# Optimization experiments

Measured on AMD Instinct MI355X. Metric: run time of the kernel, lower is better.

The kernel has to match this reference:

```python
import jax, jax.numpy as jnp
import numpy as np
from jax import lax

B, H, W = 1, 128, 128
KS = 3
N = KS * KS  # 9 deformable sampling points
BN_EPS = 1e-5


def conv2d(x, w, padding=0, stride=1):
    return lax.conv_general_dilated(x, w, (stride, stride),
                                    [(padding, padding), (padding, padding)],
                                    dimension_numbers=('NCHW', 'OIHW', 'NCHW'))


def bn_eval(x, gamma, beta, mean, var):
    scale = gamma / jnp.sqrt(var + BN_EPS)
    return x * scale[None, :, None, None] + (beta - mean * scale)[None, :, None, None]


def upsample_bilinear_ac(x, oh, ow):
    # F.interpolate(mode='bilinear', align_corners=True), separable gather
    b, c, h, w = x.shape
    ys = jnp.linspace(0.0, h - 1.0, oh)
    xs = jnp.linspace(0.0, w - 1.0, ow)
    y0 = jnp.floor(ys).astype(jnp.int32)
    y1 = jnp.minimum(y0 + 1, h - 1)
    wy = (ys - y0).astype(x.dtype)[None, None, :, None]
    x0 = jnp.floor(xs).astype(jnp.int32)
    x1 = jnp.minimum(x0 + 1, w - 1)
    wx = (xs - x0).astype(x.dtype)
    r = x[:, :, y0, :] * (1.0 - wy) + x[:, :, y1, :] * wy
    return r[:, :, :, x0] * (1.0 - wx) + r[:, :, :, x1] * wx


def deform_conv(x, p_w, p_b, dc_w, pad=1):
    # DeformConv2d(inc, outc, ks=3, padding=1, modulation=False):
    # offsets from a 3x3 conv, bilinear gather at p0 + p_n + offset on the
    # zero-padded input, then 3x3 kernel contraction over the 9 samples.
    b, c, h, w = x.shape
    off = conv2d(x, p_w, padding=1) + p_b[None, :, None, None]  # (b, 2N, h, w)
    rng = jnp.arange(KS, dtype=x.dtype) - (KS - 1) // 2          # [-1, 0, 1]
    pnx, pny = jnp.meshgrid(rng, rng, indexing='ij')
    # absolute sampling coords in padded frame, (b, h, w, N)
    px = jnp.transpose(off[:, :N], (0, 2, 3, 1)) + pnx.ravel() + jnp.arange(1, h + 1, dtype=x.dtype)[None, :, None, None]
    py = jnp.transpose(off[:, N:], (0, 2, 3, 1)) + pny.ravel() + jnp.arange(1, w + 1, dtype=x.dtype)[None, None, :, None]
    Hp, Wp = h + 2 * pad, w + 2 * pad
    xp = jnp.pad(x, ((0, 0), (0, 0), (pad, pad), (pad, pad))).reshape(b, c, Hp * Wp)
    fx = jnp.floor(px)
    fy = jnp.floor(py)
    x0f = jnp.clip(fx, 0, Hp - 1)
    x1f = jnp.clip(fx + 1.0, 0, Hp - 1)
    y0f = jnp.clip(fy, 0, Wp - 1)
    y1f = jnp.clip(fy + 1.0, 0, Wp - 1)
    pxc = jnp.clip(px, 0, Hp - 1)
    pyc = jnp.clip(py, 0, Wp - 1)

    def gather(qxf, qyf):
        idx = (qxf.astype(jnp.int32) * Wp + qyf.astype(jnp.int32)).reshape(b, 1, h * w * N)
        g = jnp.take_along_axis(xp, jnp.broadcast_to(idx, (b, c, h * w * N)), axis=2)
        return g.reshape(b, c, h, w, N)

    g_lt = (1.0 + (x0f - pxc)) * (1.0 + (y0f - pyc))
    g_rb = (1.0 - (x1f - pxc)) * (1.0 - (y1f - pyc))
    g_lb = (1.0 + (x0f - pxc)) * (1.0 - (y1f - pyc))
    g_rt = (1.0 - (x1f - pxc)) * (1.0 + (y0f - pyc))
    x_off = (g_lt[:, None] * gather(x0f, y0f) + g_rb[:, None] * gather(x1f, y1f)
             + g_lb[:, None] * gather(x0f, y1f) + g_rt[:, None] * gather(x1f, y0f))
    # conv(kernel=3, stride=3) on the rearranged samples == contraction over N
    return jnp.einsum('bchwk,ock->bohw', x_off, dc_w.reshape(dc_w.shape[0], c, N))


def _forward(x, low_level_feat, fm_w, fs_w, p_w, p_b, dc_w,
             lc1_w, bn1_gamma, bn1_beta, bn1_mean, bn1_var,
             lc2_w, bn2_gamma, bn2_beta, bn2_mean, bn2_var):
    xu = upsample_bilinear_ac(x, H, W)                       # (B,256,128,128)
    Z = low_level_feat                                       # AdaptiveAvgPool2d((128,128)) is identity on 128x128 input
    v = jax.nn.sigmoid(jnp.einsum('oc,bchw->bohw', fm_w, Z))
    u = jnp.einsum('bchk,bckw->bchw', low_level_feat, v) + low_level_feat
    Cf = jnp.einsum('oc,bchw->bohw', fs_w, u)
    cc = jnp.concatenate([xu, Cf], axis=1)                   # (B,512,128,128)
    fam = deform_conv(cc, p_w, p_b, dc_w) + Cf
    up1 = jax.nn.relu(bn_eval(conv2d(fam, lc1_w, padding=1), bn1_gamma, bn1_beta, bn1_mean, bn1_var))
    up2 = jax.nn.relu(bn_eval(conv2d(up1, lc2_w, padding=1), bn2_gamma, bn2_beta, bn2_mean, bn2_var))
    return up1, up2


def setup_inputs():
    key = jax.random.key(0)
    ks = jax.random.split(key, 12)
    f32 = jnp.float32
    return {
        'x': jax.random.normal(ks[0], (B, 256, 32, 32), f32),
        'low_level_feat': jax.random.normal(ks[1], (B, 256, H, W), f32),
        'fm_w': jax.random.normal(ks[2], (256, 256), f32) * 0.0625,
        'fs_w': jax.random.normal(ks[3], (256, 256), f32) * 0.0625,
        'p_w': jax.random.normal(ks[4], (2 * N, 512, 3, 3), f32) * 0.01,
        'p_b': jnp.zeros((2 * N,), f32),
        'dc_w': jax.random.normal(ks[5], (256, 512, 3, 3), f32) * 0.02,
        'lc1_w': jax.random.normal(ks[6], (256, 256, 3, 3), f32) * 0.02,
        'bn1_gamma': jnp.ones((256,), f32),
        'bn1_beta': jnp.zeros((256,), f32),
        'bn1_mean': jax.random.normal(ks[7], (256,), f32) * 0.1,
        'bn1_var': jax.random.uniform(ks[8], (256,), f32) + 0.5,
        'lc2_w': jax.random.normal(ks[9], (256, 256, 3, 3), f32) * 0.02,
        'bn2_gamma': jnp.ones((256,), f32),
        'bn2_beta': jnp.zeros((256,), f32),
        'bn2_mean': jax.random.normal(ks[10], (256,), f32) * 0.1,
        'bn2_var': jax.random.uniform(ks[11], (256,), f32) + 0.5,
    }


def reference(x, low_level_feat, fm_w, fs_w, p_w, p_b, dc_w,
              lc1_w, bn1_gamma, bn1_beta, bn1_mean, bn1_var,
              lc2_w, bn2_gamma, bn2_beta, bn2_mean, bn2_var):
    return _forward(x, low_level_feat, fm_w, fs_w, p_w, p_b, dc_w,
                    lc1_w, bn1_gamma, bn1_beta, bn1_mean, bn1_var,
                    lc2_w, bn2_gamma, bn2_beta, bn2_mean, bn2_var)
```

## Files before the change

### kernel.cpp

```cpp
#include <hip/hip_runtime.h>
#include <math.h>

#define HW   16384
#define PS   16900

typedef __attribute__((ext_vector_type(8))) short bf16x8;
typedef __attribute__((ext_vector_type(4))) float f32x4;

__device__ inline unsigned short f2bf(float x) {
    unsigned int u = __float_as_uint(x);
    unsigned int r = (u + 0x7fffu + ((u >> 16) & 1u)) >> 16;
    return (unsigned short)r;
}
__device__ inline float bf2f(unsigned short h) {
    return __uint_as_float(((unsigned int)h) << 16);
}

__global__ __launch_bounds__(256) void zero_ringP_k(unsigned short* __restrict__ base) {
    int t = blockIdx.x * 256 + threadIdx.x;
    if (t >= 520 * 32) return;
    int ck = (t & 31) << 3, rp = t >> 5;
    int row, col;
    if (rp < 130)      { row = 0;   col = rp; }
    else if (rp < 260) { row = 129; col = rp - 130; }
    else {
        int rem = rp - 260;
        if (rem >= 256) return;
        row = 1 + (rem >> 1); col = (rem & 1) ? 129 : 0;
    }
    bf16x8 z = (bf16x8){0, 0, 0, 0, 0, 0, 0, 0};
    *(bf16x8*)(base + (size_t)(row * 130 + col) * 256 + ck) = z;
}

__global__ __launch_bounds__(256) void ringT_k(unsigned short* __restrict__ ccT) {
    int t = blockIdx.x * 256 + threadIdx.x;
    if (t >= 520 * 256) return;
    int ci = t & 255, rp = t >> 8;
    int row, col;
    if (rp < 130)      { row = 0;   col = rp; }
    else if (rp < 260) { row = 129; col = rp - 130; }
    else {
        int rem = rp - 260;
        if (rem >= 256) return;
        row = 1 + (rem >> 1); col = (rem & 1) ? 129 : 0;
    }
    ccT[(size_t)(row * 130 + col) * 512 + 256 + ci] = 0;
}

__global__ __launch_bounds__(256) void upsample_k(const float* __restrict__ x,
                                                  float* __restrict__ ccpad) {
    int c = blockIdx.y;
    int idx = blockIdx.x * 256 + threadIdx.x;
    if (idx >= PS) return;
    int r = idx / 130, s = idx - r * 130;
    float val = 0.0f;
    if (r >= 1 && r <= 128 && s >= 1 && s <= 128) {
        int i = r - 1, j = s - 1;
        float yf = (float)i * (31.0f / 127.0f);
        float xf = (float)j * (31.0f / 127.0f);
        int y0 = min((int)yf, 31); int y1 = min(y0 + 1, 31);
        int x0 = min((int)xf, 31); int x1 = min(x0 + 1, 31);
        float wy = yf - (float)y0, wx = xf - (float)x0;
        const float* xc = x + (size_t)c * 1024;
        float a = xc[y0 * 32 + x0] * (1.0f - wx) + xc[y0 * 32 + x1] * wx;
        float b = xc[y1 * 32 + x0] * (1.0f - wx) + xc[y1 * 32 + x1] * wx;
        val = a * (1.0f - wy) + b * wy;
    }
    ccpad[(size_t)c * PS + idx] = val;
}

__global__ __launch_bounds__(256) void cvtT_flat_k(const float* __restrict__ src,
                                                   unsigned short* __restrict__ dst,
                                                   int npx) {
    int t = blockIdx.x * 256 + threadIdx.x;
    int c = t & 255, pix = t >> 8;
    dst[t] = f2bf(src[(size_t)c * npx + pix]);
}

__global__ __launch_bounds__(256) void cvtT_k(const float* __restrict__ src,
                                              unsigned short* __restrict__ dst) {
    int t = blockIdx.x * 256 + threadIdx.x;
    int c = t & 255, pix = t >> 8;
    dst[(size_t)pix * 512 + c] = f2bf(src[(size_t)c * PS + pix]);
}

__global__ __launch_bounds__(256) void w2bf_k(const float* __restrict__ a,
                                              const float* __restrict__ b,
                                              unsigned short* __restrict__ da,
                                              unsigned short* __restrict__ db) {
    int t = blockIdx.x * 256 + threadIdx.x;
    if (t >= 65536) return;
    da[t] = f2bf(a[t]);
    db[t] = f2bf(b[t]);
}

__global__ __launch_bounds__(256) void u_matmul_k(const float* __restrict__ llf,
                                                  const float* __restrict__ v,
                                                  float* __restrict__ u) {
    int c = blockIdx.y;
    const float* L = llf + (size_t)c * HW;
    const float* V = v   + (size_t)c * HW;
    float*       U = u   + (size_t)c * HW;
    int tid = threadIdx.x;
    int ty = tid >> 4, tx = tid & 15;
    int r0 = (blockIdx.x << 6) + (ty << 2);
    int w0 = tx << 3;
    float acc[4][8] = {};
    for (int k = 0; k < 128; ++k) {
        float a[4];
#pragma unroll
        for (int i = 0; i < 4; ++i) a[i] = L[(r0 + i) * 128 + k];
        float4 b0 = *(const float4*)(V + k * 128 + w0);
        float4 b1 = *(const float4*)(V + k * 128 + w0 + 4);
        float bv[8] = {b0.x, b0.y, b0.z, b0.w, b1.x, b1.y, b1.z, b1.w};
#pragma unroll
        for (int i = 0; i < 4; ++i)
#pragma unroll
            for (int j = 0; j < 8; ++j) acc[i][j] += a[i] * bv[j];
    }
#pragma unroll
    for (int i = 0; i < 4; ++i) {
#pragma unroll
        for (int j = 0; j < 8; ++j) acc[i][j] += L[(r0 + i) * 128 + w0 + j];
        *(float4*)(U + (r0 + i) * 128 + w0)     = make_float4(acc[i][0], acc[i][1], acc[i][2], acc[i][3]);
        *(float4*)(U + (r0 + i) * 128 + w0 + 4) = make_float4(acc[i][4], acc[i][5], acc[i][6], acc[i][7]);
    }
}

__global__ __launch_bounds__(256) void tr_dcwF9_k(const float* __restrict__ w,
                                                  unsigned short* __restrict__ dst) {
    int t = blockIdx.x * 256 + threadIdx.x;
    if (t >= 1179648) return;
    int e    = t & 7;
    int lane = (t >> 3) & 63;
    int f    = t >> 9;
    int mi   = f & 1;
    int s    = (f >> 1) & 1;
    int wv   = (f >> 2) & 7;
    int ch   = f >> 5;
    int kt   = ch >> 3;
    int o = (wv << 5) + (mi << 4) + (lane & 15);
    int c = ((ch & 7) << 6) + (s << 5) + ((lane >> 4) << 3) + e;
    dst[t] = f2bf(w[(size_t)o * 4608 + c * 9 + kt]);
}

__global__ __launch_bounds__(256) void tr_lcF_k(const float* __restrict__ w,
                                                unsigned short* __restrict__ dst) {
    int t = blockIdx.x * 256 + threadIdx.x;
    if (t >= 589824) return;
    int e    = t & 7;
    int lane = (t >> 3) & 63;
    int mi   = (t >> 9) & 3;
    int kss  = (t >> 11) & 7;
    int wo   = (t >> 14) & 3;
    int kt   = t >> 16;
    int o = (wo << 6) + (mi << 4) + (lane & 15);
    int c = (kss << 5) + ((lane >> 4) << 3) + e;
    dst[t] = f2bf(w[(size_t)o * 2304 + c * 9 + kt]);
}

__global__ __launch_bounds__(256) void tr_pw_k(const float* __restrict__ w,
                                               unsigned short* __restrict__ dst) {
    int t = blockIdx.x * 256 + threadIdx.x;
    if (t >= 9 * 32 * 512) return;
    int c = t & 511; int rest = t >> 9; int o = rest & 31; int k = rest >> 5;
    dst[t] = (o < 18) ? f2bf(w[(size_t)o * 4608 + c * 9 + k]) : (unsigned short)0;
}

__global__ __launch_bounds__(256, 2) void vmfma_k(
        const unsigned short* __restrict__ inT,
        const unsigned short* __restrict__ wh,
        float* __restrict__ vout) {
    __shared__ __align__(16) unsigned short Bs[32][72];
    int b = blockIdx.x;
    int xcd = b & 7, sl = b >> 3;
    int nt = (xcd << 6) + sl;
    int hrow = nt >> 2, pc0 = (nt & 3) << 5;
    int tid = threadIdx.x;
    int wv = tid >> 6, lane = tid & 63;
    int lr = lane & 15, lg = lane >> 4;
    int pxs = tid >> 3, cg8 = tid & 7;
    int p = (hrow << 7) + pc0 + pxs;
    f32x4 acc[4][2];
#pragma unroll
    for (int i = 0; i < 4; ++i)
#pragma unroll
        for (int j = 0; j < 2; ++j) acc[i][j] = (f32x4){0.f, 0.f, 0.f, 0.f};
    for (int ks = 0; ks < 256; ks += 64) {
        __syncthreads();
        *(bf16x8*)&Bs[pxs][cg8 << 3] =
            *(const bf16x8*)(inT + (size_t)p * 256 + ks + (cg8 << 3));
        __syncthreads();
#pragma unroll
        for (int s = 0; s < 2; ++s) {
            int ko = ks + (s << 5) + (lg << 3);
            bf16x8 af[4], bfr[2];
#pragma unroll
            for (int mi = 0; mi < 4; ++mi)
                af[mi] = *(const bf16x8*)(wh + (size_t)((wv << 6) + (mi << 4) + lr) * 256 + ko);
#pragma unroll
            for (int ni = 0; ni < 2; ++ni)
                bfr[ni] = *(const bf16x8*)(&Bs[(ni << 4) + lr][(s << 5) + (lg << 3)]);
#pragma unroll
            for (int mi = 0; mi < 4; ++mi)
#pragma unroll
                for (int ni = 0; ni < 2; ++ni)
                    acc[mi][ni] = __builtin_amdgcn_mfma_f32_16x16x32_bf16(
                        af[mi], bfr[ni], acc[mi][ni], 0, 0, 0);
        }
    }
#pragma unroll
    for (int mi = 0; mi < 4; ++mi)
#pragma unroll
        for (int ni = 0; ni < 2; ++ni)
#pragma unroll
            for (int r = 0; r < 4; ++r) {
                int o   = (wv << 6) + (mi << 4) + (lg << 2) + r;
                int pxx = pc0 + (ni << 4) + lr;
                vout[(size_t)o * HW + (hrow << 7) + pxx] =
                    1.0f / (1.0f + expf(-acc[mi][ni][r]));
            }
}

__global__ __launch_bounds__(256, 2) void cfmfma_k(
        const unsigned short* __restrict__ inT,
        const unsigned short* __restrict__ wh,
        unsigned short* __restrict__ ccT) {
    __shared__ __align__(16) unsigned short Bs[32][72];
    int b = blockIdx.x;
    int xcd = b & 7, sl = b >> 3;
    int nt = (xcd << 6) + sl;
    int hrow = nt >> 2, pc0 = (nt & 3) << 5;
    int tid = threadIdx.x;
    int wv = tid >> 6, lane = tid & 63;
    int lr = lane & 15, lg = lane >> 4;
    int pxs = tid >> 3, cg8 = tid & 7;
    int p = (hrow << 7) + pc0 + pxs;
    f32x4 acc[4][2];
#pragma unroll
    for (int i = 0; i < 4; ++i)
#pragma unroll
        for (int j = 0; j < 2; ++j) acc[i][j] = (f32x4){0.f, 0.f, 0.f, 0.f};
    for (int ks = 0; ks < 256; ks += 64) {
        __syncthreads();
        *(bf16x8*)&Bs[pxs][cg8 << 3] =
            *(const bf16x8*)(inT + (size_t)p * 256 + ks + (cg8 << 3));
        __syncthreads();
#pragma unroll
        for (int s = 0; s < 2; ++s) {
            int ko = ks + (s << 5) + (lg << 3);
            bf16x8 af[4], bfr[2];
#pragma unroll
            for (int mi = 0; mi < 4; ++mi)
                af[mi] = *(const bf16x8*)(wh + (size_t)((wv << 6) + (mi << 4) + lr) * 256 + ko);
#pragma unroll
            for (int ni = 0; ni < 2; ++ni)
                bfr[ni] = *(const bf16x8*)(&Bs[(ni << 4) + lr][(s << 5) + (lg << 3)]);
#pragma unroll
            for (int mi = 0; mi < 4; ++mi)
#pragma unroll
                for (int ni = 0; ni < 2; ++ni)
                    acc[mi][ni] = __builtin_amdgcn_mfma_f32_16x16x32_bf16(
                        af[mi], bfr[ni], acc[mi][ni], 0, 0, 0);
        }
    }
#pragma unroll
    for (int mi = 0; mi < 4; ++mi)
#pragma unroll
        for (int ni = 0; ni < 2; ++ni) {
            int pxx = pc0 + (ni << 4) + lr;
            int pix = (hrow + 1) * 130 + pxx + 1;
            unsigned short pk[4];
#pragma unroll
            for (int r = 0; r < 4; ++r) pk[r] = f2bf(acc[mi][ni][r]);
            *(ushort4*)(ccT + (size_t)pix * 512 + 256 + (wv << 6) + (mi << 4) + (lg << 2))
                = *(ushort4*)pk;
        }
}

__global__ __launch_bounds__(256, 2) void off_part2_k(
        const unsigned short* __restrict__ ccT,
        const unsigned short* __restrict__ pwTh,
        float* __restrict__ pbuf) {
    __shared__ __align__(16) unsigned short Ls[198][132];
    int b = blockIdx.x;
    int xcd = b & 7, slot = b >> 3;
    int hrow = (xcd << 4) + (slot >> 3);
    int rest = slot & 7;
    int pxh = rest >> 2, cg = rest & 3;
    int pc0h = pxh << 6, c0 = cg << 7;
    int tid = threadIdx.x;
    int wv = tid >> 6, lane = tid & 63;
    int lr = lane & 15, lg = lane >> 4;
    int wo = wv & 1;
    int pt0 = (wv >> 1) << 1;
    int chk = tid & 15, pxi0 = tid >> 4;
#pragma unroll
    for (int r = 0; r < 3; ++r) {
        const unsigned short* src = ccT + (size_t)((hrow + r) * 130 + pc0h) * 512 + c0;
        for (int pxi = pxi0; pxi < 66; pxi += 16)
            *(bf16x8*)&Ls[r * 66 + pxi][chk << 3] =
                *(const bf16x8*)(src + (size_t)pxi * 512 + (chk << 3));
    }
    __syncthreads();

    f32x4 acc[2];
    acc[0] = (f32x4){0.f, 0.f, 0.f, 0.f};
    acc[1] = (f32x4){0.f, 0.f, 0.f, 0.f};
    for (int kt = 0; kt < 9; ++kt) {
        int rowb = (kt / 3) * 66 + (kt % 3);
        const unsigned short* wk = pwTh + (size_t)kt * 16384
                                 + (size_t)((wo << 4) + lr) * 512 + c0;
#pragma unroll
        for (int ks = 0; ks < 128; ks += 32) {
            bf16x8 af = *(const bf16x8*)(wk + ks + (lg << 3));
#pragma unroll
            for (int pi = 0; pi < 2; ++pi) {
                int px = ((pt0 + pi) << 4) + lr;
                bf16x8 bfr = *(const bf16x8*)(&Ls[rowb + px][ks + (lg << 3)]);
                acc[pi] = __builtin_amdgcn_mfma_f32_16x16x32_bf16(af, bfr, acc[pi], 0, 0, 0);
            }
        }
    }
#pragma unroll
    for (int pi = 0; pi < 2; ++pi)
#pragma unroll
        for (int r = 0; r < 4; ++r) {
            int o = (wo << 4) + (lg << 2) + r;
            int p = (hrow << 7) + pc0h + ((pt0 + pi) << 4) + lr;
            pbuf[(size_t)((cg << 5) + o) * HW + p] = acc[pi][r];
        }
}

__global__ __launch_bounds__(256) void make_idx_k(const float* __restrict__ pbuf,
                                                  const float* __restrict__ pb,
                                                  int4* __restrict__ IDX,
                                                  float4* __restrict__ WT) {
    int t = blockIdx.x * 256 + threadIdx.x;
    if (t >= 9 * HW) return;
    int k = t >> 14, p = t & 16383;
    int h = p >> 7, w = p & 127;
    float ox = 0.f, oy = 0.f;
#pragma unroll
    for (int cg = 0; cg < 4; ++cg) {
        ox += pbuf[(size_t)((cg << 5) + k) * HW + p];
        oy += pbuf[(size_t)((cg << 5) + 9 + k) * HW + p];
    }
    float px = ox + pb[k]     + (float)(k / 3 - 1) + (float)(h + 1);
    float py = oy + pb[9 + k] + (float)(k % 3 - 1) + (float)(w + 1);
    float fx = floorf(px), fy = floorf(py);
    float x0 = fminf(fmaxf(fx,        0.f), 129.f);
    float x1 = fminf(fmaxf(fx + 1.0f, 0.f), 129.f);
    float y0 = fminf(fmaxf(fy,        0.f), 129.f);
    float y1 = fminf(fmaxf(fy + 1.0f, 0.f), 129.f);
    float pxc = fminf(fmaxf(px, 0.f), 129.f);
    float pyc = fminf(fmaxf(py, 0.f), 129.f);
    float gx0 = 1.0f + x0 - pxc, gx1 = 1.0f - x1 + pxc;
    float gy0 = 1.0f + y0 - pyc, gy1 = 1.0f - y1 + pyc;
    int ix0 = (int)x0, ix1 = (int)x1, iy0 = (int)y0, iy1 = (int)y1;
    IDX[t] = make_int4((ix0 * 130 + iy0) << 9, (ix1 * 130 + iy1) << 9,
                       (ix0 * 130 + iy1) << 9, (ix1 * 130 + iy0) << 9);
    WT[t]  = make_float4(gx0 * gy0, gx1 * gy1, gx0 * gy1, gx1 * gy0);
}

__global__ __launch_bounds__(512, 4) void fam9_k(
        const unsigned short* __restrict__ ccT,
        const unsigned short* __restrict__ dcwF,
        const int4* __restrict__ IDX, const float4* __restrict__ WT,
        unsigned short* __restrict__ part0,
        unsigned short* __restrict__ part1) {
    __shared__ __align__(16) unsigned short Bs[2][64][72];
    int b = blockIdx.x;
    int khalf = b >> 8;
    int bb = b & 255;
    int xcd = bb & 7, sl = bb >> 3;
    int nt = (xcd << 5) + sl;
    int hrow = nt >> 1, pc0 = (nt & 1) << 6;
    int tid = threadIdx.x;
    int wv = tid >> 6, lane = tid & 63;
    int lr = lane & 15, lg = lane >> 4;
    int pxg = tid >> 3, grp = tid & 7;
    int p2 = (hrow << 7) + pc0 + pxg;
    const unsigned short* wfb = dcwF + ((size_t)wv << 11) + ((size_t)lane << 3);
    f32x4 acc[2][4];
#pragma unroll
    for (int i = 0; i < 2; ++i)
#pragma unroll
        for (int j = 0; j < 4; ++j) acc[i][j] = (f32x4){0.f, 0.f, 0.f, 0.f};

    bf16x8 v0, v1, v2, v3;
    bf16x8 Aa00, Aa01, Aa10, Aa11;
    bf16x8 Ba00, Ba01, Ba10, Ba11;

#define ISSUE_A9(S, ch) do {                                                  \
    const unsigned short* ap_ = wfb + ((size_t)(ch) << 14);                   \
    S##00 = *(const bf16x8*)(ap_);                                            \
    S##01 = *(const bf16x8*)(ap_ + 512);                                      \
    S##10 = *(const bf16x8*)(ap_ + 1024);                                     \
    S##11 = *(const bf16x8*)(ap_ + 1536);                                     \
} while (0)

#define ISSUE_G9(ch, idm) do {                                                \
    int cb_ = (((ch) & 7) << 6) + (grp << 3);                                 \
    v0 = *(const bf16x8*)(ccT + (idm).x + cb_);                               \
    v1 = *(const bf16x8*)(ccT + (idm).y + cb_);                               \
    v2 = *(const bf16x8*)(ccT + (idm).z + cb_);                               \
    v3 = *(const bf16x8*)(ccT + (idm).w + cb_);                               \
} while (0)

#define NEXT_G9(cn) do {                                                      \
    if ((cn) < c1) {                                                          \
        if (((cn) & 7) == 0) {                                                \
            idc = idn; wtc = wtn;                                             \
            int kt2_ = ((cn) >> 3) + 1;                                       \
            if ((kt2_ << 3) < c1) {                                           \
                idn = IDX[(kt2_ << 14) + p2];                                 \
                wtn = WT [(kt2_ << 14) + p2];                                 \
            }                                                                 \
        }                                                                     \
        ISSUE_G9(cn, idc);                                                    \
        wnext = wtc;                                                          \
    }                                                                         \
} while (0)

#define PUBLISH9(bi) do {                                                     \
    unsigned short pk_[8];                                                    \
    _Pragma("unroll")                                                         \
    for (int e_ = 0; e_ < 8; ++e_) {                                          \
        float val_ = wcur.x * bf2f((unsigned short)v0[e_])                    \
                   + wcur.y * bf2f((unsigned short)v1[e_])                    \
                   + wcur.z * bf2f((unsigned short)v2[e_])                    \
                   + wcur.w * bf2f((unsigned short)v3[e_]);                   \
        pk_[e_] = f2bf(val_);                                                 \
    }                                                                         \
    *(bf16x8*)&Bs[bi][pxg][grp << 3] = *(bf16x8*)pk_;                         \
} while (0)

#define MFMA9(S, bi) do {                                                     \
    _Pragma("unroll")                                                         \
    for (int ni_ = 0; ni_ < 4; ++ni_) {                                       \
        bf16x8 b0_ = *(const bf16x8*)(&Bs[bi][(ni_ << 4) + lr][lg << 3]);     \
        acc[0][ni_] = __builtin_amdgcn_mfma_f32_16x16x32_bf16(S##00, b0_, acc[0][ni_], 0, 0, 0); \
        acc[1][ni_] = __builtin_amdgcn_mfma_f32_16x16x32_bf16(S##01, b0_, acc[1][ni_], 0, 0, 0); \
    }                                                                         \
    _Pragma("unroll")                                                         \
    for (int ni_ = 0; ni_ < 4; ++ni_) {                                       \
        bf16x8 b1_ = *(const bf16x8*)(&Bs[bi][(ni_ << 4) + lr][32 + (lg << 3)]); \
        acc[0][ni_] = __builtin_amdgcn_mfma_f32_16x16x32_bf16(S##10, b1_, acc[0][ni_], 0, 0, 0); \
        acc[1][ni_] = __builtin_amdgcn_mfma_f32_16x16x32_bf16(S##11, b1_, acc[1][ni_], 0, 0, 0); \
    }                                                                         \
} while (0)

    int c0 = khalf * 36, c1 = c0 + 36;
    int kt0 = c0 >> 3;
    int4   idc = IDX[(kt0 << 14) + p2];
    float4 wtc = WT [(kt0 << 14) + p2];
    int4   idn = IDX[((kt0 + 1) << 14) + p2];
    float4 wtn = WT [((kt0 + 1) << 14) + p2];
    ISSUE_G9(c0, idc);
    float4 wcur = wtc, wnext = wtc;
    ISSUE_A9(Aa, c0);

    for (int c = c0; c < c1; c += 2) {
        PUBLISH9(0);
        NEXT_G9(c + 1);
        ISSUE_A9(Ba, c + 1);
        __syncthreads();
        MFMA9(Aa, 0);
        wcur = wnext;
        PUBLISH9(1);
        NEXT_G9(c + 2);
        if (c + 2 < c1) ISSUE_A9(Aa, c + 2);
        __syncthreads();
        MFMA9(Ba, 1);
        wcur = wnext;
    }
#undef ISSUE_A9
#undef ISSUE_G9
#undef NEXT_G9
#undef PUBLISH9
#undef MFMA9

    unsigned short* pt = khalf ? part1 : part0;
#pragma unroll
    for (int mi = 0; mi < 2; ++mi)
#pragma unroll
        for (int ni = 0; ni < 4; ++ni) {
            int pxx = pc0 + (ni << 4) + lr;
            int p = (hrow << 7) + pxx;
            unsigned short pk[4];
#pragma unroll
            for (int r = 0; r < 4; ++r) pk[r] = f2bf(acc[mi][ni][r]);
            *(ushort4*)(pt + (size_t)p * 256 + (wv << 5) + (mi << 4) + (lg << 2))
                = *(ushort4*)pk;
        }
}

__global__ __launch_bounds__(256) void combineT_k(
        const unsigned short* __restrict__ p0,
        const unsigned short* __restrict__ p1,
        const unsigned short* __restrict__ ccT,
        unsigned short* __restrict__ famT) {
    int t = blockIdx.x * 256 + threadIdx.x;
    int o8 = (t & 31) << 3, p = t >> 5;
    int row = p >> 7, col = p & 127;
    int pix = (row + 1) * 130 + col + 1;
    bf16x8 a = *(const bf16x8*)(p0 + (size_t)p * 256 + o8);
    bf16x8 b = *(const bf16x8*)(p1 + (size_t)p * 256 + o8);
    bf16x8 c = *(const bf16x8*)(ccT + (size_t)pix * 512 + 256 + o8);
    unsigned short out[8];
#pragma unroll
    for (int e = 0; e < 8; ++e)
        out[e] = f2bf(bf2f((unsigned short)a[e]) + bf2f((unsigned short)b[e])
                      + bf2f((unsigned short)c[e]));
    *(bf16x8*)(famT + (size_t)pix * 256 + o8) = *(bf16x8*)out;
}

__global__ __launch_bounds__(256, 2) void conv2T_k(
        const unsigned short* __restrict__ inT,
        const unsigned short* __restrict__ wF,
        const float* __restrict__ gam, const float* __restrict__ bet,
        const float* __restrict__ mean, const float* __restrict__ var,
        float* __restrict__ out_flat,
        unsigned short* __restrict__ out_padT) {
    __shared__ __align__(16) unsigned short Ls[102][264];
    __shared__ float scs[256], bis[256];
    int b = blockIdx.x;
    int xcd = b & 7, slot = b >> 3;
    int nt = (xcd << 6) + slot;
    int hrow = nt >> 2, pc0 = (nt & 3) << 5;
    int tid = threadIdx.x;
    int wv = tid >> 6, lane = tid & 63;
    int lr = lane & 15, lg = lane >> 4;
    {
        float sc = gam[tid] * rsqrtf(var[tid] + 1e-5f);
        scs[tid] = sc;
        bis[tid] = bet[tid] - mean[tid] * sc;
    }
#pragma unroll
    for (int r = 0; r < 3; ++r) {
        const unsigned short* src = inT + (size_t)((hrow + r) * 130 + pc0) * 256;
#pragma unroll
        for (int ps = 0; ps < 5; ++ps) {
            int idx = ps * 2048 + tid * 8;
            if (idx < 8704) {
                bf16x8 v = *(const bf16x8*)(src + idx);
                *(bf16x8*)&Ls[r * 34 + (idx >> 8)][idx & 255] = v;
            }
        }
    }
    __syncthreads();

    f32x4 acc[4][2];
#pragma unroll
    for (int i = 0; i < 4; ++i)
#pragma unroll
        for (int j = 0; j < 2; ++j) acc[i][j] = (f32x4){0.f, 0.f, 0.f, 0.f};

    const unsigned short* wvb = wF + ((size_t)wv << 14) + ((size_t)lane << 3);
    for (int kt = 0; kt < 9; ++kt) {
        int rowb = (kt / 3) * 34 + (kt % 3);
        const unsigned short* wkb = wvb + (size_t)kt * 65536;
#pragma unroll
        for (int kss = 0; kss < 8; ++kss) {
            int ks = kss << 5;
            bf16x8 af[4], bfr[2];
#pragma unroll
            for (int mi = 0; mi < 4; ++mi)
                af[mi] = *(const bf16x8*)(wkb + (size_t)kss * 2048 + mi * 512);
#pragma unroll
            for (int ni = 0; ni < 2; ++ni)
                bfr[ni] = *(const bf16x8*)(&Ls[rowb + (ni << 4) + lr][ks + (lg << 3)]);
#pragma unroll
            for (int mi = 0; mi < 4; ++mi)
#pragma unroll
                for (int ni = 0; ni < 2; ++ni)
                    acc[mi][ni] = __builtin_amdgcn_mfma_f32_16x16x32_bf16(
                        af[mi], bfr[ni], acc[mi][ni], 0, 0, 0);
        }
    }

#pragma unroll
    for (int mi = 0; mi < 4; ++mi)
#pragma unroll
        for (int ni = 0; ni < 2; ++ni) {
            int pxx = pc0 + (ni << 4) + lr;
            unsigned short pk[4];
#pragma unroll
            for (int r = 0; r < 4; ++r) {
                int o = (wv << 6) + (mi << 4) + (lg << 2) + r;
                float rv = fmaxf(acc[mi][ni][r] * scs[o] + bis[o], 0.0f);
                out_flat[(size_t)o * HW + (hrow << 7) + pxx] = rv;
                pk[r] = f2bf(rv);
            }
            if (out_padT) {
                int pix = (hrow + 1) * 130 + pxx + 1;
                *(ushort4*)(out_padT + (size_t)pix * 256 + (wv << 6) + (mi << 4) + (lg << 2))
                    = *(ushort4*)pk;
            }
        }
}

extern "C" void kernel_launch(void* const* d_in, const int* in_sizes, int n_in,
                              void* d_out, int out_size, void* d_ws, size_t ws_size,
                              hipStream_t stream) {
    const float* x     = (const float*)d_in[0];
    const float* llf   = (const float*)d_in[1];
    const float* fm_w  = (const float*)d_in[2];
    const float* fs_w  = (const float*)d_in[3];
    const float* p_w   = (const float*)d_in[4];
    const float* p_b   = (const float*)d_in[5];
    const float* dc_w  = (const float*)d_in[6];
    const float* lc1_w = (const float*)d_in[7];
    const float* bn1g  = (const float*)d_in[8];
    const float* bn1b  = (const float*)d_in[9];
    const float* bn1m  = (const float*)d_in[10];
    const float* bn1v  = (const float*)d_in[11];
    const float* lc2_w = (const float*)d_in[12];
    const float* bn2g  = (const float*)d_in[13];
    const float* bn2b  = (const float*)d_in[14];
    const float* bn2m  = (const float*)d_in[15];
    const float* bn2v  = (const float*)d_in[16];
    float* out1 = (float*)d_out;
    float* out2 = out1 + (size_t)256 * HW;

    if (ws_size < 79839232u) return;
    char* ws = (char*)d_ws;
    unsigned short* ccT   = (unsigned short*)ws;
    float*          ccpad = (float*)(ws + 17305600);
    float*          vbuf  = (float*)(ws + 17305600);
    unsigned short* famT  = (unsigned short*)(ws + 17305600);
    unsigned short* up1T  = (unsigned short*)(ws + 26091520);
    unsigned short* llfT  = (unsigned short*)(ws + 34877440);
    unsigned short* uT    = (unsigned short*)(ws + 43266048);
    unsigned short* part0 = (unsigned short*)(ws + 43266048);
    unsigned short* fmwh  = (unsigned short*)(ws + 51654656);
    unsigned short* fswh  = (unsigned short*)(ws + 51785728);
    float*          ubuf  = (float*)(ws + 51916800);
    float*          pbuf  = (float*)(ws + 51916800);
    unsigned short* part1 = (unsigned short*)(ws + 51916800);
    int4*           IDX   = (int4*)  (ws + 60305408);
    float4*         WT    = (float4*)(ws + 62664704);
    unsigned short* dcwF   = (unsigned short*)(ws + 68694016);
    unsigned short* lcw1F  = (unsigned short*)(ws + 71053312);
    unsigned short* lcw2F  = (unsigned short*)(ws + 72232960);
    unsigned short* pwTh   = (unsigned short*)(ws + 73412608);

    upsample_k<<<dim3(67, 256), 256, 0, stream>>>(x, ccpad);
    cvtT_k<<<dim3(16900), 256, 0, stream>>>(ccpad, ccT);
    cvtT_flat_k<<<dim3(16384), 256, 0, stream>>>(llf, llfT, HW);
    w2bf_k<<<dim3(256), 256, 0, stream>>>(fm_w, fs_w, fmwh, fswh);
    vmfma_k<<<dim3(512), 256, 0, stream>>>(llfT, fmwh, vbuf);
    u_matmul_k<<<dim3(2, 256), 256, 0, stream>>>(llf, vbuf, ubuf);
    cvtT_flat_k<<<dim3(16384), 256, 0, stream>>>(ubuf, uT, HW);
    tr_dcwF9_k<<<dim3(4608), 256, 0, stream>>>(dc_w, dcwF);
    tr_lcF_k<<<dim3(2304), 256, 0, stream>>>(lc1_w, lcw1F);
    tr_lcF_k<<<dim3(2304), 256, 0, stream>>>(lc2_w, lcw2F);
    tr_pw_k<<<dim3(576), 256, 0, stream>>>(p_w, pwTh);
    cfmfma_k<<<dim3(512), 256, 0, stream>>>(uT, fswh, ccT);
    ringT_k<<<dim3(520), 256, 0, stream>>>(ccT);
    off_part2_k<<<dim3(1024), 256, 0, stream>>>(ccT, pwTh, pbuf);
    make_idx_k<<<dim3(576), 256, 0, stream>>>(pbuf, p_b, IDX, WT);
    zero_ringP_k<<<dim3(65), 256, 0, stream>>>(famT);
    zero_ringP_k<<<dim3(65), 256, 0, stream>>>(up1T);
    fam9_k<<<dim3(512), 512, 0, stream>>>(ccT, dcwF, IDX, WT, part0, part1);
    combineT_k<<<dim3(2048), 256, 0, stream>>>(part0, part1, ccT, famT);
    conv2T_k<<<dim3(512), 256, 0, stream>>>(famT, lcw1F, bn1g, bn1b, bn1m, bn1v,
                                            out1, up1T);
    conv2T_k<<<dim3(512), 256, 0, stream>>>(up1T, lcw2F, bn2g, bn2b, bn2m, bn2v,
                                            out2, nullptr);
}
```

Before: 456.5 us.

## Fuse upsample with bf16 transpose, tile transposes via LDS, merge small launches

Replaces the upsample-to-fp32-padded-buffer plus strided transpose with a small channel-last copy of x and a fused kernel that interpolates and writes bf16 channel-last directly. The naive strided transposes of llf and u become LDS-tiled transposes with coalesced reads and 16-byte vector writes. The two ring-zeroing launches and the two lc weight-reformat launches are each merged into one. This targets uncoalesced global traffic and launch overhead in the preprocessing stages, at the cost of an extra small xT buffer and more complex indexing.

```diff
diff --git a/kernel.cpp b/kernel.cpp
--- a/kernel.cpp
+++ b/kernel.cpp
@@ -16,10 +16,13 @@
     return __uint_as_float(((unsigned int)h) << 16);
 }
 
-__global__ __launch_bounds__(256) void zero_ringP_k(unsigned short* __restrict__ base) {
-    int t = blockIdx.x * 256 + threadIdx.x;
-    if (t >= 520 * 32) return;
-    int ck = (t & 31) << 3, rp = t >> 5;
+__global__ __launch_bounds__(256) void zero_ringP2_k(unsigned short* __restrict__ b0,
+                                                     unsigned short* __restrict__ b1) {
+    int t = blockIdx.x * 256 + threadIdx.x;
+    if (t >= 2 * 520 * 32) return;
+    unsigned short* base = (t >= 520 * 32) ? b1 : b0;
+    int tt = (t >= 520 * 32) ? t - 520 * 32 : t;
+    int ck = (tt & 31) << 3, rp = tt >> 5;
     int row, col;
     if (rp < 130)      { row = 0;   col = rp; }
     else if (rp < 260) { row = 129; col = rp - 130; }
@@ -47,12 +50,18 @@
     ccT[(size_t)(row * 130 + col) * 512 + 256 + ci] = 0;
 }
 
-__global__ __launch_bounds__(256) void upsample_k(const float* __restrict__ x,
-                                                  float* __restrict__ ccpad) {
-    int c = blockIdx.y;
-    int idx = blockIdx.x * 256 + threadIdx.x;
-    if (idx >= PS) return;
-    int r = idx / 130, s = idx - r * 130;
+__global__ __launch_bounds__(256) void xT_k(const float* __restrict__ x,
+                                            float* __restrict__ xT) {
+    int t = blockIdx.x * 256 + threadIdx.x;
+    int c = t & 255, pos = t >> 8;
+    xT[t] = x[(size_t)c * 1024 + pos];
+}
+
+__global__ __launch_bounds__(256) void up_cvtT_k(const float* __restrict__ xT,
+                                                 unsigned short* __restrict__ ccT) {
+    int pix = blockIdx.x;
+    int c = threadIdx.x;
+    int r = pix / 130, s = pix - r * 130;
     float val = 0.0f;
     if (r >= 1 && r <= 128 && s >= 1 && s <= 128) {
         int i = r - 1, j = s - 1;
@@ -61,27 +70,40 @@
         int y0 = min((int)yf, 31); int y1 = min(y0 + 1, 31);
         int x0 = min((int)xf, 31); int x1 = min(x0 + 1, 31);
         float wy = yf - (float)y0, wx = xf - (float)x0;
-        const float* xc = x + (size_t)c * 1024;
-        float a = xc[y0 * 32 + x0] * (1.0f - wx) + xc[y0 * 32 + x1] * wx;
-        float b = xc[y1 * 32 + x0] * (1.0f - wx) + xc[y1 * 32 + x1] * wx;
+        float v00 = xT[(size_t)(y0 * 32 + x0) * 256 + c];
+        float v01 = xT[(size_t)(y0 * 32 + x1) * 256 + c];
+        float v10 = xT[(size_t)(y1 * 32 + x0) * 256 + c];
+        float v11 = xT[(size_t)(y1 * 32 + x1) * 256 + c];
+        float a = v00 * (1.0f - wx) + v01 * wx;
+        float b = v10 * (1.0f - wx) + v11 * wx;
         val = a * (1.0f - wy) + b * wy;
     }
-    ccpad[(size_t)c * PS + idx] = val;
-}
-
-__global__ __launch_bounds__(256) void cvtT_flat_k(const float* __restrict__ src,
-                                                   unsigned short* __restrict__ dst,
-                                                   int npx) {
-    int t = blockIdx.x * 256 + threadIdx.x;
-    int c = t & 255, pix = t >> 8;
-    dst[t] = f2bf(src[(size_t)c * npx + pix]);
-}
-
-__global__ __launch_bounds__(256) void cvtT_k(const float* __restrict__ src,
-                                              unsigned short* __restrict__ dst) {
-    int t = blockIdx.x * 256 + threadIdx.x;
-    int c = t & 255, pix = t >> 8;
-    dst[(size_t)pix * 512 + c] = f2bf(src[(size_t)c * PS + pix]);
+    ccT[(size_t)pix * 512 + c] = f2bf(val);
+}
+
+__global__ __launch_bounds__(256) void cvtT_tile_k(const float* __restrict__ src,
+                                                   unsigned short* __restrict__ dst) {
+    __shared__ float Ls[64][65];
+    int px0 = blockIdx.x << 6;
+    int c0  = blockIdx.y << 6;
+    int t = threadIdx.x;
+    int pxl = t & 63, cq = t >> 6;
+#pragma unroll
+    for (int it = 0; it < 16; ++it) {
+        int cl = (it << 2) + cq;
+        Ls[cl][pxl] = src[(size_t)(c0 + cl) * HW + px0 + pxl];
+    }
+    __syncthreads();
+    int c8 = (t & 7) << 3;
+    int pxb = t >> 3;
+#pragma unroll
+    for (int rr = 0; rr < 2; ++rr) {
+        int px = pxb + (rr << 5);
+        unsigned short pk[8];
+#pragma unroll
+        for (int e = 0; e < 8; ++e) pk[e] = f2bf(Ls[c8 + e][px]);
+        *(bf16x8*)(dst + (size_t)(px0 + px) * 256 + c0 + c8) = *(bf16x8*)pk;
+    }
 }
 
 __global__ __launch_bounds__(256) void w2bf_k(const float* __restrict__ a,
@@ -144,8 +166,12 @@
     dst[t] = f2bf(w[(size_t)o * 4608 + c * 9 + kt]);
 }
 
-__global__ __launch_bounds__(256) void tr_lcF_k(const float* __restrict__ w,
-                                                unsigned short* __restrict__ dst) {
+__global__ __launch_bounds__(256) void tr_lcF2_k(const float* __restrict__ w1,
+                                                 const float* __restrict__ w2,
+                                                 unsigned short* __restrict__ d1,
+                                                 unsigned short* __restrict__ d2) {
+    const float* w = blockIdx.y ? w2 : w1;
+    unsigned short* dst = blockIdx.y ? d2 : d1;
     int t = blockIdx.x * 256 + threadIdx.x;
     if (t >= 589824) return;
     int e    = t & 7;
@@ -627,7 +653,7 @@
     if (ws_size < 79839232u) return;
     char* ws = (char*)d_ws;
     unsigned short* ccT   = (unsigned short*)ws;
-    float*          ccpad = (float*)(ws + 17305600);
+    float*          xTf   = (float*)(ws + 17305600);
     float*          vbuf  = (float*)(ws + 17305600);
     unsigned short* famT  = (unsigned short*)(ws + 17305600);
     unsigned short* up1T  = (unsigned short*)(ws + 26091520);
@@ -646,23 +672,21 @@
     unsigned short* lcw2F  = (unsigned short*)(ws + 72232960);
     unsigned short* pwTh   = (unsigned short*)(ws + 73412608);
 
-    upsample_k<<<dim3(67, 256), 256, 0, stream>>>(x, ccpad);
-    cvtT_k<<<dim3(16900), 256, 0, stream>>>(ccpad, ccT);
-    cvtT_flat_k<<<dim3(16384), 256, 0, stream>>>(llf, llfT, HW);
+    xT_k<<<dim3(1024), 256, 0, stream>>>(x, xTf);
+    up_cvtT_k<<<dim3(16900), 256, 0, stream>>>(xTf, ccT);
+    cvtT_tile_k<<<dim3(256, 4), 256, 0, stream>>>(llf, llfT);
     w2bf_k<<<dim3(256), 256, 0, stream>>>(fm_w, fs_w, fmwh, fswh);
     vmfma_k<<<dim3(512), 256, 0, stream>>>(llfT, fmwh, vbuf);
     u_matmul_k<<<dim3(2, 256), 256, 0, stream>>>(llf, vbuf, ubuf);
-    cvtT_flat_k<<<dim3(16384), 256, 0, stream>>>(ubuf, uT, HW);
+    cvtT_tile_k<<<dim3(256, 4), 256, 0, stream>>>(ubuf, uT);
     tr_dcwF9_k<<<dim3(4608), 256, 0, stream>>>(dc_w, dcwF);
-    tr_lcF_k<<<dim3(2304), 256, 0, stream>>>(lc1_w, lcw1F);
-    tr_lcF_k<<<dim3(2304), 256, 0, stream>>>(lc2_w, lcw2F);
+    tr_lcF2_k<<<dim3(2304, 2), 256, 0, stream>>>(lc1_w, lc2_w, lcw1F, lcw2F);
     tr_pw_k<<<dim3(576), 256, 0, stream>>>(p_w, pwTh);
     cfmfma_k<<<dim3(512), 256, 0, stream>>>(uT, fswh, ccT);
     ringT_k<<<dim3(520), 256, 0, stream>>>(ccT);
     off_part2_k<<<dim3(1024), 256, 0, stream>>>(ccT, pwTh, pbuf);
     make_idx_k<<<dim3(576), 256, 0, stream>>>(pbuf, p_b, IDX, WT);
-    zero_ringP_k<<<dim3(65), 256, 0, stream>>>(famT);
-    zero_ringP_k<<<dim3(65), 256, 0, stream>>>(up1T);
+    zero_ringP2_k<<<dim3(130), 256, 0, stream>>>(famT, up1T);
     fam9_k<<<dim3(512), 512, 0, stream>>>(ccT, dcwF, IDX, WT, part0, part1);
     combineT_k<<<dim3(2048), 256, 0, stream>>>(part0, part1, ccT, famT);
     conv2T_k<<<dim3(512), 256, 0, stream>>>(famT, lcw1F, bn1g, bn1b, bn1m, bn1v,
```

Result: faster. 396.8 us (-13.1%).
